# Performance work log

Hardware: AMD Instinct MI355X
Metric: run time of the kernel (lower is better)

## Reference

```python
import jax, jax.numpy as jnp
import numpy as np
import math

B, H, S, D = 2, 16, 2048, 64

def setup_inputs() -> dict:
    key = jax.random.key(0)
    kq, kk, kv = jax.random.split(key, 3)
    Q = jax.random.normal(kq, (B, H, S, D), dtype=jnp.float32)
    K = jax.random.normal(kk, (B, H, S, D), dtype=jnp.float32)
    V = jax.random.normal(kv, (B, H, S, D), dtype=jnp.float32)
    attn_mask = jnp.ones((B, 1, S, S), dtype=jnp.int32)
    return {"Q": Q, "K": K, "V": V, "attn_mask": attn_mask}

def reference(Q, K, V, attn_mask):
    # scores: [B, H, S, S]
    scores = jnp.einsum('bhqd,bhkd->bhqk', Q, K) / math.sqrt(D)
    scores = jnp.where(attn_mask == 0, jnp.float32(-1e9), scores)
    attn_prob = jax.nn.softmax(scores, axis=-1)
    # dropout p=0.0 (eval): identity
    context = jnp.einsum('bhqk,bhkd->bhqd', attn_prob, V)
    return (context, attn_prob)
```

## Files before the change

kernel.cpp:

```cpp
#include <hip/hip_runtime.h>
#include <math.h>

constexpr int Bc = 2, Hc = 16, Sc = 2048, Dc = 64;
constexpr int BM = 64;
constexpr int BN = 64;
constexpr int LDQ = 72;
constexpr int LDV = 72;
constexpr int NKT = Sc / BN;
constexpr float SCALE = 0.125f;

typedef __bf16 bf16_t;
typedef __bf16 bf16x8 __attribute__((ext_vector_type(8)));
typedef __bf16 bf16x4 __attribute__((ext_vector_type(4)));
typedef float floatx4 __attribute__((ext_vector_type(4)));

#define MFMA16(a, b, c) __builtin_amdgcn_mfma_f32_16x16x32_bf16((a), (b), (c), 0, 0, 0)

__global__ __launch_bounds__(256, 2)
void sdpa_fused_kernel(const float* __restrict__ Q, const float* __restrict__ K,
                       const float* __restrict__ V, const int* __restrict__ Mask,
                       float* __restrict__ CtxOut, float* __restrict__ ProbOut)
{
    __shared__ __align__(16) bf16_t Qs[BM * LDQ];
    __shared__ __align__(16) bf16_t Ks[BN * LDQ];
    __shared__ __align__(16) bf16_t Vt[Dc * LDV];
    __shared__ __align__(16) bf16_t Ps[BM * LDQ];

    const int tid  = threadIdx.x;
    const int wave = tid >> 6;
    const int lane = tid & 63;
    const int quad = lane >> 4;
    const int l16  = lane & 15;

    const int qt    = blockIdx.x;
    const int bh    = blockIdx.y;
    const int b     = bh >> 4;
    const int qbase = qt * BM;

    const float* Qp = Q + ((size_t)bh * Sc + qbase) * Dc;
    const float* Kp = K + (size_t)bh * Sc * Dc;
    const float* Vp = V + (size_t)bh * Sc * Dc;
    const int*   Mp = Mask + (size_t)b * Sc * Sc;
    float* Pg = ProbOut + (size_t)bh * Sc * Sc;
    float* Cg = CtxOut + ((size_t)bh * Sc + qbase) * Dc;

    #pragma unroll
    for (int t = 0; t < 4; ++t) {
        int i = tid + t * 256;
        int r = i >> 4;
        int c = (i & 15) << 2;
        float4 v = *reinterpret_cast<const float4*>(Qp + r * Dc + c);
        bf16x4 w; w[0] = (bf16_t)v.x; w[1] = (bf16_t)v.y; w[2] = (bf16_t)v.z; w[3] = (bf16_t)v.w;
        *reinterpret_cast<bf16x4*>(&Qs[r * LDQ + c]) = w;
    }
    __syncthreads();

    const int qrow_lds = wave * 16 + l16;
    bf16x8 qa0 = *reinterpret_cast<const bf16x8*>(&Qs[qrow_lds * LDQ + quad * 8]);
    bf16x8 qa1 = *reinterpret_cast<const bf16x8*>(&Qs[qrow_lds * LDQ + 32 + quad * 8]);

    float m_i[4], l_i[4];
    #pragma unroll
    for (int r = 0; r < 4; ++r) { m_i[r] = -3.0e38f; l_i[r] = 0.f; }

    const int mrow0 = qbase + wave * 16 + quad * 4;
    const int* mr[4]; float* pr[4];
    #pragma unroll
    for (int r = 0; r < 4; ++r) {
        mr[r] = Mp + (size_t)(mrow0 + r) * Sc;
        pr[r] = Pg + (size_t)(mrow0 + r) * Sc;
    }

    float4 kreg[4];
    #pragma unroll
    for (int t = 0; t < 4; ++t) {
        int i = tid + t * 256;
        kreg[t] = *reinterpret_cast<const float4*>(Kp + (i >> 4) * Dc + ((i & 15) << 2));
    }
    for (int kt = 0; kt < NKT; ++kt) {
        __syncthreads();
        #pragma unroll
        for (int t = 0; t < 4; ++t) {
            int i = tid + t * 256;
            int r = i >> 4;
            int c = (i & 15) << 2;
            bf16x4 w; w[0] = (bf16_t)kreg[t].x; w[1] = (bf16_t)kreg[t].y;
                      w[2] = (bf16_t)kreg[t].z; w[3] = (bf16_t)kreg[t].w;
            *reinterpret_cast<bf16x4*>(&Ks[r * LDQ + c]) = w;
        }
        if (kt + 1 < NKT) {
            const float* Kn = Kp + (size_t)(kt + 1) * BN * Dc;
            #pragma unroll
            for (int t = 0; t < 4; ++t) {
                int i = tid + t * 256;
                kreg[t] = *reinterpret_cast<const float4*>(Kn + (i >> 4) * Dc + ((i & 15) << 2));
            }
        }
        __syncthreads();

        const int kc = kt * BN + l16;
        int mv[4][4];
        #pragma unroll
        for (int nt = 0; nt < 4; ++nt)
            #pragma unroll
            for (int r = 0; r < 4; ++r)
                mv[nt][r] = mr[r][kc + nt * 16];

        floatx4 acc[4];
        #pragma unroll
        for (int nt = 0; nt < 4; ++nt) acc[nt] = (floatx4){0.f, 0.f, 0.f, 0.f};
        #pragma unroll
        for (int nt = 0; nt < 4; ++nt) {
            const bf16_t* kr = &Ks[(nt * 16 + l16) * LDQ + quad * 8];
            bf16x8 kb0 = *reinterpret_cast<const bf16x8*>(kr);
            bf16x8 kb1 = *reinterpret_cast<const bf16x8*>(kr + 32);
            acc[nt] = MFMA16(qa0, kb0, acc[nt]);
            acc[nt] = MFMA16(qa1, kb1, acc[nt]);
        }
        #pragma unroll
        for (int nt = 0; nt < 4; ++nt) {
            #pragma unroll
            for (int r = 0; r < 4; ++r) {
                float sv = acc[nt][r] * SCALE;
                acc[nt][r] = mv[nt][r] ? sv : -1e9f;
            }
        }
        #pragma unroll
        for (int r = 0; r < 4; ++r) {
            float mx = fmaxf(fmaxf(acc[0][r], acc[1][r]), fmaxf(acc[2][r], acc[3][r]));
            #pragma unroll
            for (int off = 1; off < 16; off <<= 1) mx = fmaxf(mx, __shfl_xor(mx, off, 64));
            float mn = fmaxf(m_i[r], mx);
            float sum = __expf(acc[0][r] - mn) + __expf(acc[1][r] - mn) +
                        __expf(acc[2][r] - mn) + __expf(acc[3][r] - mn);
            #pragma unroll
            for (int off = 1; off < 16; off <<= 1) sum += __shfl_xor(sum, off, 64);
            l_i[r] = l_i[r] * __expf(m_i[r] - mn) + sum;
            m_i[r] = mn;
        }
    }

    float linv[4];
    #pragma unroll
    for (int r = 0; r < 4; ++r) linv[r] = 1.0f / l_i[r];

    floatx4 co[4];
    #pragma unroll
    for (int dt = 0; dt < 4; ++dt) co[dt] = (floatx4){0.f, 0.f, 0.f, 0.f};

    float4 vreg[4];
    #pragma unroll
    for (int t = 0; t < 4; ++t) {
        int i = tid + t * 256;
        kreg[t] = *reinterpret_cast<const float4*>(Kp + (i >> 4) * Dc + ((i & 15) << 2));
        vreg[t] = *reinterpret_cast<const float4*>(Vp + (size_t)lane * Dc + 4 * (4 * wave + t));
    }
    for (int kt = 0; kt < NKT; ++kt) {
        __syncthreads();
        #pragma unroll
        for (int t = 0; t < 4; ++t) {
            int i = tid + t * 256;
            int r = i >> 4;
            int c = (i & 15) << 2;
            bf16x4 w; w[0] = (bf16_t)kreg[t].x; w[1] = (bf16_t)kreg[t].y;
                      w[2] = (bf16_t)kreg[t].z; w[3] = (bf16_t)kreg[t].w;
            *reinterpret_cast<bf16x4*>(&Ks[r * LDQ + c]) = w;
            const int d0 = 4 * (4 * wave + t);
            Vt[(d0 + 0) * LDV + lane] = (bf16_t)vreg[t].x;
            Vt[(d0 + 1) * LDV + lane] = (bf16_t)vreg[t].y;
            Vt[(d0 + 2) * LDV + lane] = (bf16_t)vreg[t].z;
            Vt[(d0 + 3) * LDV + lane] = (bf16_t)vreg[t].w;
        }
        if (kt + 1 < NKT) {
            const float* Kn = Kp + (size_t)(kt + 1) * BN * Dc;
            const float* Vn = Vp + (size_t)(kt + 1) * BN * Dc;
            #pragma unroll
            for (int t = 0; t < 4; ++t) {
                int i = tid + t * 256;
                kreg[t] = *reinterpret_cast<const float4*>(Kn + (i >> 4) * Dc + ((i & 15) << 2));
                vreg[t] = *reinterpret_cast<const float4*>(Vn + (size_t)lane * Dc + 4 * (4 * wave + t));
            }
        }
        __syncthreads();

        const int kc = kt * BN + l16;
        int mv[4][4];
        #pragma unroll
        for (int nt = 0; nt < 4; ++nt)
            #pragma unroll
            for (int r = 0; r < 4; ++r)
                mv[nt][r] = mr[r][kc + nt * 16];

        floatx4 acc[4];
        #pragma unroll
        for (int nt = 0; nt < 4; ++nt) acc[nt] = (floatx4){0.f, 0.f, 0.f, 0.f};
        #pragma unroll
        for (int nt = 0; nt < 4; ++nt) {
            const bf16_t* kr = &Ks[(nt * 16 + l16) * LDQ + quad * 8];
            bf16x8 kb0 = *reinterpret_cast<const bf16x8*>(kr);
            bf16x8 kb1 = *reinterpret_cast<const bf16x8*>(kr + 32);
            acc[nt] = MFMA16(qa0, kb0, acc[nt]);
            acc[nt] = MFMA16(qa1, kb1, acc[nt]);
        }
        #pragma unroll
        for (int nt = 0; nt < 4; ++nt) {
            #pragma unroll
            for (int r = 0; r < 4; ++r) {
                float sv = acc[nt][r] * SCALE;
                sv = mv[nt][r] ? sv : -1e9f;
                float p = __expf(sv - m_i[r]) * linv[r];
                pr[r][kc + nt * 16] = p;
                Ps[(wave * 16 + quad * 4 + r) * LDQ + nt * 16 + l16] = (bf16_t)p;
            }
        }
        #pragma unroll
        for (int ks = 0; ks < 2; ++ks) {
            bf16x8 pa = *reinterpret_cast<const bf16x8*>(
                &Ps[(wave * 16 + l16) * LDQ + ks * 32 + quad * 8]);
            #pragma unroll
            for (int dt = 0; dt < 4; ++dt) {
                bf16x8 vb = *reinterpret_cast<const bf16x8*>(
                    &Vt[(dt * 16 + l16) * LDV + ks * 32 + quad * 8]);
                co[dt] = MFMA16(pa, vb, co[dt]);
            }
        }
    }

    #pragma unroll
    for (int dt = 0; dt < 4; ++dt) {
        #pragma unroll
        for (int r = 0; r < 4; ++r) {
            Cg[(size_t)(wave * 16 + quad * 4 + r) * Dc + dt * 16 + l16] = co[dt][r];
        }
    }
}

extern "C" void kernel_launch(void* const* d_in, const int* in_sizes, int n_in,
                              void* d_out, int out_size, void* d_ws, size_t ws_size,
                              hipStream_t stream) {
    const float* Q    = (const float*)d_in[0];
    const float* K    = (const float*)d_in[1];
    const float* V    = (const float*)d_in[2];
    const int*   mask = (const int*)d_in[3];

    float* ctx  = (float*)d_out;
    float* prob = (float*)d_out + (size_t)Bc * Hc * Sc * Dc;

    dim3 grid(Sc / BM, Bc * Hc);
    sdpa_fused_kernel<<<grid, 256, 0, stream>>>(Q, K, V, mask, ctx, prob);
}
```

Measured before the change: 855.3 us.

## Double-buffer K/V LDS tiles with XOR swizzle and load Q directly to registers

Replaces the padded single-buffered K and V^T shared tiles with double-buffered tiles using an XOR swizzle instead of padding. Each iteration now needs one barrier instead of two, and the next tile is written to LDS while the current one is being consumed. Q is loaded straight from global memory into MFMA registers, so the Q LDS staging and its barrier go away. The kernel is likely bound by the large probability-matrix writes, so these changes may have limited effect, and the larger LDS footprint could affect occupancy.

Result: faster. 836.0 us (-2.3%).

```diff
diff --git a/kernel.cpp b/kernel.cpp
--- a/kernel.cpp
+++ b/kernel.cpp
@@ -4,9 +4,8 @@
 constexpr int Bc = 2, Hc = 16, Sc = 2048, Dc = 64;
 constexpr int BM = 64;
 constexpr int BN = 64;
-constexpr int LDQ = 72;
-constexpr int LDV = 72;
 constexpr int NKT = Sc / BN;
+constexpr int TS  = BN * Dc;
 constexpr float SCALE = 0.125f;
 
 typedef __bf16 bf16_t;
@@ -15,16 +14,19 @@
 typedef float floatx4 __attribute__((ext_vector_type(4)));
 
 #define MFMA16(a, b, c) __builtin_amdgcn_mfma_f32_16x16x32_bf16((a), (b), (c), 0, 0, 0)
+
+__device__ __forceinline__ int swzi(int row, int byteoff) {
+    return row * 64 + ((byteoff ^ ((row & 7) << 4)) >> 1);
+}
 
 __global__ __launch_bounds__(256, 2)
 void sdpa_fused_kernel(const float* __restrict__ Q, const float* __restrict__ K,
                        const float* __restrict__ V, const int* __restrict__ Mask,
                        float* __restrict__ CtxOut, float* __restrict__ ProbOut)
 {
-    __shared__ __align__(16) bf16_t Qs[BM * LDQ];
-    __shared__ __align__(16) bf16_t Ks[BN * LDQ];
-    __shared__ __align__(16) bf16_t Vt[Dc * LDV];
-    __shared__ __align__(16) bf16_t Ps[BM * LDQ];
+    __shared__ bf16_t Ks[2 * TS];
+    __shared__ bf16_t Vt[2 * TS];
+    __shared__ bf16_t Ps[TS];
 
     const int tid  = threadIdx.x;
     const int wave = tid >> 6;
@@ -44,20 +46,47 @@
     float* Pg = ProbOut + (size_t)bh * Sc * Sc;
     float* Cg = CtxOut + ((size_t)bh * Sc + qbase) * Dc;
 
+    const float* qrow = Qp + (size_t)(wave * 16 + l16) * Dc;
+    float4 qv0 = *reinterpret_cast<const float4*>(qrow + quad * 8);
+    float4 qv1 = *reinterpret_cast<const float4*>(qrow + quad * 8 + 4);
+    float4 qv2 = *reinterpret_cast<const float4*>(qrow + 32 + quad * 8);
+    float4 qv3 = *reinterpret_cast<const float4*>(qrow + 32 + quad * 8 + 4);
+    bf16x8 qa0, qa1;
+    qa0[0]=(bf16_t)qv0.x; qa0[1]=(bf16_t)qv0.y; qa0[2]=(bf16_t)qv0.z; qa0[3]=(bf16_t)qv0.w;
+    qa0[4]=(bf16_t)qv1.x; qa0[5]=(bf16_t)qv1.y; qa0[6]=(bf16_t)qv1.z; qa0[7]=(bf16_t)qv1.w;
+    qa1[0]=(bf16_t)qv2.x; qa1[1]=(bf16_t)qv2.y; qa1[2]=(bf16_t)qv2.z; qa1[3]=(bf16_t)qv2.w;
+    qa1[4]=(bf16_t)qv3.x; qa1[5]=(bf16_t)qv3.y; qa1[6]=(bf16_t)qv3.z; qa1[7]=(bf16_t)qv3.w;
+
+    int srow[4], sbyte[4];
     #pragma unroll
     for (int t = 0; t < 4; ++t) {
         int i = tid + t * 256;
-        int r = i >> 4;
-        int c = (i & 15) << 2;
-        float4 v = *reinterpret_cast<const float4*>(Qp + r * Dc + c);
-        bf16x4 w; w[0] = (bf16_t)v.x; w[1] = (bf16_t)v.y; w[2] = (bf16_t)v.z; w[3] = (bf16_t)v.w;
-        *reinterpret_cast<bf16x4*>(&Qs[r * LDQ + c]) = w;
-    }
-    __syncthreads();
-
-    const int qrow_lds = wave * 16 + l16;
-    bf16x8 qa0 = *reinterpret_cast<const bf16x8*>(&Qs[qrow_lds * LDQ + quad * 8]);
-    bf16x8 qa1 = *reinterpret_cast<const bf16x8*>(&Qs[qrow_lds * LDQ + 32 + quad * 8]);
+        srow[t]  = i >> 4;
+        sbyte[t] = (i & 15) << 3;
+    }
+    const int vd0 = 16 * wave;
+
+#define LOADK(kt_) { const float* Kt_ = Kp + (size_t)(kt_) * (BN * Dc);                      \
+    _Pragma("unroll") for (int t = 0; t < 4; ++t)                                            \
+        kreg[t] = *reinterpret_cast<const float4*>(Kt_ + srow[t] * Dc + (sbyte[t] >> 1)); }
+#define WRITEK(buf_) { _Pragma("unroll") for (int t = 0; t < 4; ++t) {                       \
+    bf16x4 w; w[0]=(bf16_t)kreg[t].x; w[1]=(bf16_t)kreg[t].y;                                \
+              w[2]=(bf16_t)kreg[t].z; w[3]=(bf16_t)kreg[t].w;                                \
+    *reinterpret_cast<bf16x4*>(&Ks[(buf_) * TS + swzi(srow[t], sbyte[t])]) = w; } }
+#define LOADV(kt_) { const float* Vt_ = Vp + (size_t)(kt_) * (BN * Dc);                      \
+    _Pragma("unroll") for (int t = 0; t < 4; ++t)                                            \
+        vreg[t] = *reinterpret_cast<const float4*>(Vt_ + (size_t)lane * Dc + vd0 + 4 * t); }
+#define WRITEV(buf_) { _Pragma("unroll") for (int t = 0; t < 4; ++t) { int d0 = vd0 + 4 * t; \
+    Vt[(buf_) * TS + swzi(d0 + 0, lane * 2)] = (bf16_t)vreg[t].x;                            \
+    Vt[(buf_) * TS + swzi(d0 + 1, lane * 2)] = (bf16_t)vreg[t].y;                            \
+    Vt[(buf_) * TS + swzi(d0 + 2, lane * 2)] = (bf16_t)vreg[t].z;                            \
+    Vt[(buf_) * TS + swzi(d0 + 3, lane * 2)] = (bf16_t)vreg[t].w; } }
+#define QK_MFMA(cur_) { _Pragma("unroll") for (int nt = 0; nt < 4; ++nt) {                   \
+    const int krow_ = nt * 16 + l16;                                                         \
+    bf16x8 kb0 = *reinterpret_cast<const bf16x8*>(&Ks[(cur_) * TS + swzi(krow_, quad * 16)]);\
+    bf16x8 kb1 = *reinterpret_cast<const bf16x8*>(&Ks[(cur_) * TS + swzi(krow_, quad * 16 + 64)]); \
+    acc[nt] = MFMA16(qa0, kb0, acc[nt]);                                                     \
+    acc[nt] = MFMA16(qa1, kb1, acc[nt]); } }
 
     float m_i[4], l_i[4];
     #pragma unroll
@@ -72,33 +101,15 @@
     }
 
     float4 kreg[4];
-    #pragma unroll
-    for (int t = 0; t < 4; ++t) {
-        int i = tid + t * 256;
-        kreg[t] = *reinterpret_cast<const float4*>(Kp + (i >> 4) * Dc + ((i & 15) << 2));
-    }
+    LOADK(0);
+    WRITEK(0);
+    LOADK(1);
+    __syncthreads();
+
     for (int kt = 0; kt < NKT; ++kt) {
-        __syncthreads();
-        #pragma unroll
-        for (int t = 0; t < 4; ++t) {
-            int i = tid + t * 256;
-            int r = i >> 4;
-            int c = (i & 15) << 2;
-            bf16x4 w; w[0] = (bf16_t)kreg[t].x; w[1] = (bf16_t)kreg[t].y;
-                      w[2] = (bf16_t)kreg[t].z; w[3] = (bf16_t)kreg[t].w;
-            *reinterpret_cast<bf16x4*>(&Ks[r * LDQ + c]) = w;
-        }
-        if (kt + 1 < NKT) {
-            const float* Kn = Kp + (size_t)(kt + 1) * BN * Dc;
-            #pragma unroll
-            for (int t = 0; t < 4; ++t) {
-                int i = tid + t * 256;
-                kreg[t] = *reinterpret_cast<const float4*>(Kn + (i >> 4) * Dc + ((i & 15) << 2));
-            }
-        }
-        __syncthreads();
-
-        const int kc = kt * BN + l16;
+        const int cur = kt & 1;
+        const int kc  = kt * BN + l16;
+
         int mv[4][4];
         #pragma unroll
         for (int nt = 0; nt < 4; ++nt)
@@ -109,14 +120,13 @@
         floatx4 acc[4];
         #pragma unroll
         for (int nt = 0; nt < 4; ++nt) acc[nt] = (floatx4){0.f, 0.f, 0.f, 0.f};
-        #pragma unroll
-        for (int nt = 0; nt < 4; ++nt) {
-            const bf16_t* kr = &Ks[(nt * 16 + l16) * LDQ + quad * 8];
-            bf16x8 kb0 = *reinterpret_cast<const bf16x8*>(kr);
-            bf16x8 kb1 = *reinterpret_cast<const bf16x8*>(kr + 32);
-            acc[nt] = MFMA16(qa0, kb0, acc[nt]);
-            acc[nt] = MFMA16(qa1, kb1, acc[nt]);
-        }
+        QK_MFMA(cur);
+
+        if (kt + 1 < NKT) {
+            WRITEK(cur ^ 1);
+            if (kt + 2 < NKT) LOADK(kt + 2);
+        }
+
         #pragma unroll
         for (int nt = 0; nt < 4; ++nt) {
             #pragma unroll
@@ -138,6 +148,7 @@
             l_i[r] = l_i[r] * __expf(m_i[r] - mn) + sum;
             m_i[r] = mn;
         }
+        __syncthreads();
     }
 
     float linv[4];
@@ -149,41 +160,15 @@
     for (int dt = 0; dt < 4; ++dt) co[dt] = (floatx4){0.f, 0.f, 0.f, 0.f};
 
     float4 vreg[4];
-    #pragma unroll
-    for (int t = 0; t < 4; ++t) {
-        int i = tid + t * 256;
-        kreg[t] = *reinterpret_cast<const float4*>(Kp + (i >> 4) * Dc + ((i & 15) << 2));
-        vreg[t] = *reinterpret_cast<const float4*>(Vp + (size_t)lane * Dc + 4 * (4 * wave + t));
-    }
+    LOADK(0); LOADV(0);
+    WRITEK(0); WRITEV(0);
+    LOADK(1); LOADV(1);
+    __syncthreads();
+
     for (int kt = 0; kt < NKT; ++kt) {
-        __syncthreads();
-        #pragma unroll
-        for (int t = 0; t < 4; ++t) {
-            int i = tid + t * 256;
-            int r = i >> 4;
-            int c = (i & 15) << 2;
-            bf16x4 w; w[0] = (bf16_t)kreg[t].x; w[1] = (bf16_t)kreg[t].y;
-                      w[2] = (bf16_t)kreg[t].z; w[3] = (bf16_t)kreg[t].w;
-            *reinterpret_cast<bf16x4*>(&Ks[r * LDQ + c]) = w;
-            const int d0 = 4 * (4 * wave + t);
-            Vt[(d0 + 0) * LDV + lane] = (bf16_t)vreg[t].x;
-            Vt[(d0 + 1) * LDV + lane] = (bf16_t)vreg[t].y;
-            Vt[(d0 + 2) * LDV + lane] = (bf16_t)vreg[t].z;
-            Vt[(d0 + 3) * LDV + lane] = (bf16_t)vreg[t].w;
-        }
-        if (kt + 1 < NKT) {
-            const float* Kn = Kp + (size_t)(kt + 1) * BN * Dc;
-            const float* Vn = Vp + (size_t)(kt + 1) * BN * Dc;
-            #pragma unroll
-            for (int t = 0; t < 4; ++t) {
-                int i = tid + t * 256;
-                kreg[t] = *reinterpret_cast<const float4*>(Kn + (i >> 4) * Dc + ((i & 15) << 2));
-                vreg[t] = *reinterpret_cast<const float4*>(Vn + (size_t)lane * Dc + 4 * (4 * wave + t));
-            }
-        }
-        __syncthreads();
-
-        const int kc = kt * BN + l16;
+        const int cur = kt & 1;
+        const int kc  = kt * BN + l16;
+
         int mv[4][4];
         #pragma unroll
         for (int nt = 0; nt < 4; ++nt)
@@ -194,14 +179,14 @@
         floatx4 acc[4];
         #pragma unroll
         for (int nt = 0; nt < 4; ++nt) acc[nt] = (floatx4){0.f, 0.f, 0.f, 0.f};
-        #pragma unroll
-        for (int nt = 0; nt < 4; ++nt) {
-            const bf16_t* kr = &Ks[(nt * 16 + l16) * LDQ + quad * 8];
-            bf16x8 kb0 = *reinterpret_cast<const bf16x8*>(kr);
-            bf16x8 kb1 = *reinterpret_cast<const bf16x8*>(kr + 32);
-            acc[nt] = MFMA16(qa0, kb0, acc[nt]);
-            acc[nt] = MFMA16(qa1, kb1, acc[nt]);
-        }
+        QK_MFMA(cur);
+
+        if (kt + 1 < NKT) {
+            WRITEK(cur ^ 1);
+            WRITEV(cur ^ 1);
+            if (kt + 2 < NKT) { LOADK(kt + 2); LOADV(kt + 2); }
+        }
+
         #pragma unroll
         for (int nt = 0; nt < 4; ++nt) {
             #pragma unroll
@@ -210,20 +195,21 @@
                 sv = mv[nt][r] ? sv : -1e9f;
                 float p = __expf(sv - m_i[r]) * linv[r];
                 pr[r][kc + nt * 16] = p;
-                Ps[(wave * 16 + quad * 4 + r) * LDQ + nt * 16 + l16] = (bf16_t)p;
+                Ps[swzi(wave * 16 + quad * 4 + r, (nt * 16 + l16) * 2)] = (bf16_t)p;
             }
         }
         #pragma unroll
         for (int ks = 0; ks < 2; ++ks) {
             bf16x8 pa = *reinterpret_cast<const bf16x8*>(
-                &Ps[(wave * 16 + l16) * LDQ + ks * 32 + quad * 8]);
+                &Ps[swzi(wave * 16 + l16, ks * 64 + quad * 16)]);
             #pragma unroll
             for (int dt = 0; dt < 4; ++dt) {
                 bf16x8 vb = *reinterpret_cast<const bf16x8*>(
-                    &Vt[(dt * 16 + l16) * LDV + ks * 32 + quad * 8]);
+                    &Vt[cur * TS + swzi(dt * 16 + l16, ks * 64 + quad * 16)]);
                 co[dt] = MFMA16(pa, vb, co[dt]);
             }
         }
+        __syncthreads();
     }
 
     #pragma unroll
@@ -233,6 +219,11 @@
             Cg[(size_t)(wave * 16 + quad * 4 + r) * Dc + dt * 16 + l16] = co[dt][r];
         }
     }
+#undef LOADK
+#undef WRITEK
+#undef LOADV
+#undef WRITEV
+#undef QK_MFMA
 }
 
 extern "C" void kernel_launch(void* const* d_in, const int* in_sizes, int n_in,
```
